# Performance work log

Hardware: AMD Instinct MI355X
Metric: run time of the kernel (lower is better)

## Reference

```python
import jax, jax.numpy as jnp
import numpy as np

LEAK = 0.9
BASE_THRESH = 1.0

@jax.custom_vjp
def spike_fn(x):
    return (x >= 0).astype(x.dtype)

def _spike_fwd(x):
    return (x >= 0).astype(x.dtype), x

def _spike_bwd(x, g):
    return (g / (1.0 + 10.0 * jnp.abs(x)) ** 2,)

spike_fn.defvjp(_spike_fwd, _spike_bwd)


def setup_inputs() -> dict:
    key = jax.random.key(0)
    k1, k2, k3, k4, k5 = jax.random.split(key, 5)
    B, T, C, NC, TDA = 256, 4096, 64, 4, 50
    kin_spikes_seq = jax.random.uniform(k1, (B, T, C), dtype=jnp.float32)
    tda_features = jax.random.normal(k2, (B, TDA), dtype=jnp.float32)
    W_spatial = jax.random.normal(k3, (NC, C), dtype=jnp.float32) * 0.125
    lateral = jnp.eye(NC, dtype=jnp.float32) * 1.1 - 0.1  # 1.0 diag, -0.1 off-diag
    W_tda = jax.random.normal(k4, (NC, TDA), dtype=jnp.float32) * 0.14
    b_tda = jnp.zeros((NC,), dtype=jnp.float32)
    return {
        "kin_spikes_seq": kin_spikes_seq,
        "tda_features": tda_features,
        "W_spatial": W_spatial,
        "lateral": lateral,
        "W_tda": W_tda,
        "b_tda": b_tda,
    }


def reference(kin_spikes_seq, tda_features, W_spatial, lateral, W_tda, b_tda):
    B, T, C = kin_spikes_seq.shape
    NC = W_spatial.shape[0]
    # dynamic threshold: base + 0.3*sigmoid(Linear(tda))  -> [B, NC]
    tda_mod = jax.nn.sigmoid(tda_features @ W_tda.T + b_tda) * 0.3
    dynamic_thresh = BASE_THRESH + tda_mod
    # project all time steps at once: (x @ W_spatial.T) @ lateral  -> [B, T, NC]
    proj = jnp.einsum("btc,nc->btn", kin_spikes_seq, W_spatial) @ lateral
    proj_t = jnp.transpose(proj, (1, 0, 2))  # [T, B, NC]

    def step(mem, cur_input):
        mem = LEAK * mem + cur_input
        spikes = spike_fn(mem - dynamic_thresh)
        mem = mem * (1.0 - spikes)
        return mem, spikes

    mem0 = jnp.zeros((B, NC), dtype=kin_spikes_seq.dtype)
    _, spikes_t = jax.lax.scan(step, mem0, proj_t)  # [T, B, NC]
    return jnp.transpose(spikes_t, (1, 0, 2))  # [B, T, NC]
```

## Files before the change

kernel.cpp:

```cpp
#include <hip/hip_runtime.h>
#include <math.h>

namespace {
constexpr int T    = 4096;
constexpr int C    = 64;
constexpr int NCH  = 4;
constexpr int TDAF = 50;
constexpr double LEAK = 0.9;
constexpr int CHUNK = 256;
constexpr int WARM  = 384;
}

__global__ __launch_bounds__(256, 2)
void lif_proj3(const float* __restrict__ x,
               const float* __restrict__ Wsp,
               const float* __restrict__ lat,
               double* __restrict__ proj,
               int B)
{
  const int tid = threadIdx.x;
  const int nb  = B >> 2;
  const int b0  = (blockIdx.x % nb) << 2;
  const int t00 = (blockIdx.x / nb) << 6;
  const int stride = B * NCH;

  const int c8 = tid & 7;
  const int rr = tid >> 3;
  const int bl = rr & 3;
  const int tl = rr >> 2;

  double wA[4][4], wB[4][4];
  #pragma unroll
  for (int j = 0; j < 4; ++j) {
    const int cA = c8 * 4 + j, cB = 32 + c8 * 4 + j;
    #pragma unroll
    for (int n = 0; n < 4; ++n) {
      double sA = 0.0, sB = 0.0;
      #pragma unroll
      for (int m = 0; m < 4; ++m) {
        sA += (double)Wsp[m * C + cA] * (double)lat[m * NCH + n];
        sB += (double)Wsp[m * C + cB] * (double)lat[m * NCH + n];
      }
      wA[j][n] = sA;
      wB[j][n] = sB;
    }
  }

  const float4* gx = reinterpret_cast<const float4*>(x);
  const size_t rowbase = (size_t)(b0 + bl) * T;

  float4 va0, vb0, va1, vb1;

#define LD(IT, VA, VB)                                              \
  {                                                                 \
    const size_t r16 = (rowbase + (size_t)(t00 + (IT) * 8 + tl)) * 16; \
    VA = gx[r16 + c8];                                              \
    VB = gx[r16 + 8 + c8];                                          \
  }

#define CS(IT, VA, VB)                                              \
  {                                                                 \
    double p0 = 0.0, p1 = 0.0, p2 = 0.0, p3 = 0.0;                  \
    p0 = fma((double)VA.x, wA[0][0], p0);                           \
    p1 = fma((double)VA.x, wA[0][1], p1);                           \
    p2 = fma((double)VA.x, wA[0][2], p2);                           \
    p3 = fma((double)VA.x, wA[0][3], p3);                           \
    p0 = fma((double)VA.y, wA[1][0], p0);                           \
    p1 = fma((double)VA.y, wA[1][1], p1);                           \
    p2 = fma((double)VA.y, wA[1][2], p2);                           \
    p3 = fma((double)VA.y, wA[1][3], p3);                           \
    p0 = fma((double)VA.z, wA[2][0], p0);                           \
    p1 = fma((double)VA.z, wA[2][1], p1);                           \
    p2 = fma((double)VA.z, wA[2][2], p2);                           \
    p3 = fma((double)VA.z, wA[2][3], p3);                           \
    p0 = fma((double)VA.w, wA[3][0], p0);                           \
    p1 = fma((double)VA.w, wA[3][1], p1);                           \
    p2 = fma((double)VA.w, wA[3][2], p2);                           \
    p3 = fma((double)VA.w, wA[3][3], p3);                           \
    p0 = fma((double)VB.x, wB[0][0], p0);                           \
    p1 = fma((double)VB.x, wB[0][1], p1);                           \
    p2 = fma((double)VB.x, wB[0][2], p2);                           \
    p3 = fma((double)VB.x, wB[0][3], p3);                           \
    p0 = fma((double)VB.y, wB[1][0], p0);                           \
    p1 = fma((double)VB.y, wB[1][1], p1);                           \
    p2 = fma((double)VB.y, wB[1][2], p2);                           \
    p3 = fma((double)VB.y, wB[1][3], p3);                           \
    p0 = fma((double)VB.z, wB[2][0], p0);                           \
    p1 = fma((double)VB.z, wB[2][1], p1);                           \
    p2 = fma((double)VB.z, wB[2][2], p2);                           \
    p3 = fma((double)VB.z, wB[2][3], p3);                           \
    p0 = fma((double)VB.w, wB[3][0], p0);                           \
    p1 = fma((double)VB.w, wB[3][1], p1);                           \
    p2 = fma((double)VB.w, wB[3][2], p2);                           \
    p3 = fma((double)VB.w, wB[3][3], p3);                           \
    p0 += __shfl_xor(p0, 1, 64); p1 += __shfl_xor(p1, 1, 64);       \
    p2 += __shfl_xor(p2, 1, 64); p3 += __shfl_xor(p3, 1, 64);       \
    p0 += __shfl_xor(p0, 2, 64); p1 += __shfl_xor(p1, 2, 64);       \
    p2 += __shfl_xor(p2, 2, 64); p3 += __shfl_xor(p3, 2, 64);       \
    p0 += __shfl_xor(p0, 4, 64); p1 += __shfl_xor(p1, 4, 64);       \
    p2 += __shfl_xor(p2, 4, 64); p3 += __shfl_xor(p3, 4, 64);       \
    if (c8 < 4) {                                                   \
      const double v = (c8 == 0) ? p0 : (c8 == 1) ? p1              \
                     : (c8 == 2) ? p2 : p3;                         \
      proj[(size_t)(t00 + (IT) * 8 + tl) * stride +                 \
           (b0 + bl) * 4 + c8] = v;                                 \
    }                                                               \
  }

  LD(0, va0, vb0)
  LD(1, va1, vb1)
  CS(0, va0, vb0)
  LD(2, va0, vb0)
  CS(1, va1, vb1)
  LD(3, va1, vb1)
  CS(2, va0, vb0)
  LD(4, va0, vb0)
  CS(3, va1, vb1)
  LD(5, va1, vb1)
  CS(4, va0, vb0)
  LD(6, va0, vb0)
  CS(5, va1, vb1)
  LD(7, va1, vb1)
  CS(6, va0, vb0)
  CS(7, va1, vb1)

#undef LD
#undef CS
}

__global__ __launch_bounds__(64, 1)
void lif_scan_chunk(const double* __restrict__ proj,
                    const float* __restrict__ tda,
                    const float* __restrict__ Wtda,
                    const float* __restrict__ btda,
                    unsigned long long* __restrict__ masks,
                    int B)
{
  const int lane = threadIdx.x;
  const int nw   = (B * NCH) >> 6;
  const int wv   = blockIdx.x % nw;
  const int ck   = blockIdx.x / nw;
  const int g    = wv * 64 + lane;
  const int b    = g >> 2, n = g & 3;
  const int stride = B * NCH;
  const int t1 = ck * CHUNK;
  const int s0 = (t1 >= WARM) ? (t1 - WARM) : 0;
  const int t2 = t1 + CHUNK;

  double z = (double)btda[n];
  #pragma unroll
  for (int j = 0; j < TDAF; ++j)
    z += (double)tda[b * TDAF + j] * (double)Wtda[n * TDAF + j];
  const double th = 1.0 + 0.3 / (1.0 + exp(-z));

  double pb[8][8];
  #pragma unroll
  for (int j2 = 0; j2 < 8; ++j2)
    #pragma unroll
    for (int e = 0; e < 8; ++e)
      pb[j2][e] = proj[(size_t)(s0 + j2 * 8 + e) * stride + g];

  double pre = 0.0;
  bool sflag = true;

  for (int t0 = s0; t0 < t2; t0 += 64) {
    unsigned lo = 0u, hi = 0u;
    #pragma unroll
    for (int j2 = 0; j2 < 8; ++j2) {
      #pragma unroll
      for (int e = 0; e < 8; ++e) {
        const int k = j2 * 8 + e;
        const double p  = pb[j2][e];
        const double ac = fma(LEAK, pre, p);
        pre   = sflag ? p : ac;
        sflag = (pre >= th);
        if (k < 32) lo |= ((unsigned)sflag) << k;
        else        hi |= ((unsigned)sflag) << (k - 32);
      }
      int tt = t0 + 64 + j2 * 8;
      tt = (tt < T) ? tt : (T - 64);
      #pragma unroll
      for (int e = 0; e < 8; ++e)
        pb[j2][e] = proj[(size_t)(tt + e) * stride + g];
    }
    if (t0 >= t1)
      masks[(size_t)g * (T / 64) + (t0 >> 6)] =
          ((unsigned long long)hi << 32) | lo;
  }
}

__global__ __launch_bounds__(256)
void lif_expand(const unsigned long long* __restrict__ masks,
                float* __restrict__ out)
{
  const int tid = threadIdx.x;
  const int b   = blockIdx.x >> 2;
  const int t0  = ((blockIdx.x & 3) << 10) + tid * 4;
  const int w   = t0 >> 6;

  unsigned long long m[4];
  #pragma unroll
  for (int n = 0; n < NCH; ++n)
    m[n] = masks[(size_t)(b * 4 + n) * (T / 64) + w];

  float4* o = reinterpret_cast<float4*>(out + ((size_t)b * T + t0) * NCH);
  #pragma unroll
  for (int j = 0; j < 4; ++j) {
    const int sh = (t0 + j) & 63;
    float4 v;
    v.x = ((m[0] >> sh) & 1ull) ? 1.0f : 0.0f;
    v.y = ((m[1] >> sh) & 1ull) ? 1.0f : 0.0f;
    v.z = ((m[2] >> sh) & 1ull) ? 1.0f : 0.0f;
    v.w = ((m[3] >> sh) & 1ull) ? 1.0f : 0.0f;
    o[j] = v;
  }
}

__global__ __launch_bounds__(128, 2)
void lif_proj(const float* __restrict__ x, const float* __restrict__ Wsp,
              const float* __restrict__ lat, double* __restrict__ proj, int B)
{
  __shared__ float  xl[32 * 76];
  __shared__ double wl[NCH * C];
  __shared__ double pl[8 * 17];

  const int tid = threadIdx.x;
  const int nb  = B >> 2;
  const int bq  = blockIdx.x % nb;
  const int tq  = blockIdx.x / nb;
  const int b0  = bq << 2;
  const int t00 = tq << 6;
  const int stride = B * NCH;

  #pragma unroll
  for (int k = 0; k < 2; ++k) {
    const int idx = tid + 128 * k;
    const int c = idx >> 2, n = idx & 3;
    double s = 0.0;
    #pragma unroll
    for (int m = 0; m < NCH; ++m)
      s += (double)Wsp[m * C + c] * (double)lat[m * NCH + n];
    wl[n * C + c] = s;
  }
  __syncthreads();

  const int n  = tid & 3;
  const int rr = tid >> 2;
  const int bb = rr >> 3, ii = rr & 7;

  double w[C];
  #pragma unroll
  for (int j = 0; j < C; ++j) w[j] = wl[n * C + j];

  const float4* gx = reinterpret_cast<const float4*>(x);

  for (int ch = 0; ch < 8; ++ch) {
    const int t0 = t00 + (ch << 3);
    __syncthreads();
    #pragma unroll
    for (int k = 0; k < 4; ++k) {
      const int f   = tid + 128 * k;
      const int row = f >> 4, c4 = f & 15;
      const int wb  = row >> 3, wi = row & 7;
      *reinterpret_cast<float4*>(&xl[row * 76 + c4 * 4]) =
          gx[((size_t)(b0 + wb) * T + (t0 + wi)) * 16 + c4];
    }
    __syncthreads();
    const float* rowp = &xl[rr * 76];
    double a0 = 0.0, a1 = 0.0;
    #pragma unroll
    for (int q = 0; q < 16; ++q) {
      const float4 v = *reinterpret_cast<const float4*>(&rowp[4 * q]);
      a0 = fma((double)v.x, w[4 * q + 0], a0);
      a1 = fma((double)v.y, w[4 * q + 1], a1);
      a0 = fma((double)v.z, w[4 * q + 2], a0);
      a1 = fma((double)v.w, w[4 * q + 3], a1);
    }
    pl[ii * 17 + bb * 4 + n] = a0 + a1;
    __syncthreads();
    {
      const int i = tid >> 4, c = tid & 15;
      proj[(size_t)(t0 + i) * stride + b0 * 4 + c] = pl[i * 17 + c];
    }
  }
}

__global__ __launch_bounds__(64)
void lif_scan_lds(const double* __restrict__ proj,
                  const float* __restrict__ tda,
                  const float* __restrict__ Wtda,
                  const float* __restrict__ btda,
                  float* __restrict__ out, int B)
{
  __shared__ float slds[64 * 65];
  const int lane = threadIdx.x;
  const int g = blockIdx.x * 64 + lane;
  const int b = g >> 2, n = g & 3;
  const int b0 = (blockIdx.x * 64) >> 2;
  const int stride = B * NCH;
  double z = (double)btda[n];
  #pragma unroll
  for (int j = 0; j < TDAF; ++j)
    z += (double)tda[b * TDAF + j] * (double)Wtda[n * TDAF + j];
  const double th = 1.0 + 0.3 / (1.0 + exp(-z));
  double pb[8][8];
  #pragma unroll
  for (int j2 = 0; j2 < 8; ++j2)
    #pragma unroll
    for (int e = 0; e < 8; ++e)
      pb[j2][e] = proj[(size_t)(j2 * 8 + e) * stride + g];
  double pre = 0.0;
  bool sflag = true;
  for (int t0 = 0; t0 < T; t0 += 64) {
    #pragma unroll
    for (int j2 = 0; j2 < 8; ++j2) {
      #pragma unroll
      for (int e = 0; e < 8; ++e) {
        const double p  = pb[j2][e];
        const double ac = fma(LEAK, pre, p);
        pre   = sflag ? p : ac;
        sflag = (pre >= th);
        slds[(j2 * 8 + e) * 65 + lane] = sflag ? 1.0f : 0.0f;
      }
      int tt = t0 + 64 + j2 * 8;
      tt = (tt < T) ? tt : (T - 64);
      #pragma unroll
      for (int e = 0; e < 8; ++e)
        pb[j2][e] = proj[(size_t)(tt + e) * stride + g];
    }
    __syncthreads();
    #pragma unroll
    for (int bb = 0; bb < 16; ++bb) {
      #pragma unroll
      for (int h = 0; h < 4; ++h) {
        const int flat = lane + 64 * h;
        const int i = flat >> 2, nn = flat & 3;
        out[((size_t)(b0 + bb) * T + (t0 + i)) * NCH + nn] =
            slds[i * 65 + bb * 4 + nn];
      }
    }
    __syncthreads();
  }
}

namespace fb {
constexpr int TT = 128, NT = T / TT, XPAD = 76, THREADS = 512;
}
__global__ __launch_bounds__(fb::THREADS, 2)
void lif_fused(const float* __restrict__ x, const float* __restrict__ tda,
               const float* __restrict__ Wsp, const float* __restrict__ lat,
               const float* __restrict__ Wtda, const float* __restrict__ btda,
               float* __restrict__ out)
{
  using namespace fb;
  __shared__ float  xl[2][TT * XPAD];
  __shared__ double wl[NCH * C];
  __shared__ double projl[TT * NCH];
  __shared__ float  spikel[TT * NCH];
  __shared__ double thl[NCH];
  const int b = blockIdx.x, tid = threadIdx.x;
  const int n = tid & 3, tl = tid >> 2;
  if (tid < NCH) {
    double z = (double)btda[tid];
    for (int j = 0; j < TDAF; ++j)
      z += (double)tda[b * TDAF + j] * (double)Wtda[tid * TDAF + j];
    thl[tid] = 1.0 + 0.3 / (1.0 + exp(-z));
  }
  if (tid < NCH * C) {
    const int c = tid >> 2, nn = tid & 3;
    double s = 0.0;
    for (int m = 0; m < NCH; ++m)
      s += (double)Wsp[m * C + c] * (double)lat[m * NCH + nn];
    wl[nn * C + c] = s;
  }
  __syncthreads();
  double w[C];
  #pragma unroll
  for (int j = 0; j < C; ++j) w[j] = wl[n * C + j];
  const double th = thl[n];
  const float4* gx = reinterpret_cast<const float4*>(x) + (size_t)b * (T * C / 4);
  float4 ra[4], rb[4];
  #pragma unroll
  for (int r = 0; r < 4; ++r) ra[r] = gx[tid + THREADS * r];
  double pre = 0.0;
  bool sflag = true;
  auto stage = [&](int buf, const float4* rr) {
    #pragma unroll
    for (int r = 0; r < 4; ++r) {
      const int f = tid + THREADS * r;
      const int t = f >> 4, c4 = (f & 15) << 2;
      *reinterpret_cast<float4*>(&xl[buf][t * XPAD + c4]) = rr[r];
    }
  };
  auto prefetch = [&](int k, float4* rr) {
    const float4* src = gx + (size_t)k * (TT * C / 4);
    #pragma unroll
    for (int r = 0; r < 4; ++r) rr[r] = src[tid + THREADS * r];
  };
  auto tilework = [&](int buf, int k) {
    __syncthreads();
    const float* row = &xl[buf][tl * XPAD];
    double a0 = 0.0, a1 = 0.0;
    #pragma unroll
    for (int q = 0; q < 16; ++q) {
      const float4 v = *reinterpret_cast<const float4*>(&row[4 * q]);
      a0 = fma((double)v.x, w[4 * q + 0], a0);
      a1 = fma((double)v.y, w[4 * q + 1], a1);
      a0 = fma((double)v.z, w[4 * q + 2], a0);
      a1 = fma((double)v.w, w[4 * q + 3], a1);
    }
    projl[tid] = a0 + a1;
    __syncthreads();
    if (tid < NCH) {
      #pragma unroll 4
      for (int t = 0; t < TT; ++t) {
        const double p  = projl[t * NCH + tid];
        const double ac = fma(LEAK, pre, p);
        pre   = sflag ? p : ac;
        sflag = (pre >= th);
        spikel[t * NCH + tid] = sflag ? 1.0f : 0.0f;
      }
    }
    __syncthreads();
    out[((size_t)b * T + (size_t)k * TT) * NCH + tid] = spikel[tid];
  };
  for (int k = 0; k < NT; k += 2) {
    stage(0, ra);
    if (k + 1 < NT) prefetch(k + 1, rb);
    tilework(0, k);
    stage(1, rb);
    if (k + 2 < NT) prefetch(k + 2, ra);
    tilework(1, k + 1);
  }
}

extern "C" void kernel_launch(void* const* d_in, const int* in_sizes, int n_in,
                              void* d_out, int out_size, void* d_ws, size_t ws_size,
                              hipStream_t stream) {
  const float* x    = (const float*)d_in[0];
  const float* tda  = (const float*)d_in[1];
  const float* Wsp  = (const float*)d_in[2];
  const float* lat  = (const float*)d_in[3];
  const float* Wtda = (const float*)d_in[4];
  const float* btda = (const float*)d_in[5];
  float* out = (float*)d_out;
  const int B = in_sizes[0] / (T * C);

  const size_t need_proj = (size_t)T * (size_t)B * NCH * sizeof(double);
  const size_t need_mask = (size_t)B * NCH * (T / 64) * sizeof(unsigned long long);

  if (ws_size >= need_proj + need_mask && (B % 4) == 0 && (B * NCH) % 64 == 0) {
    double* proj = (double*)d_ws;
    unsigned long long* masks =
        (unsigned long long*)((char*)d_ws + need_proj);
    lif_proj3<<<(B / 4) * (T / 64), 256, 0, stream>>>(x, Wsp, lat, proj, B);
    const int grid2 = (T / CHUNK) * ((B * NCH) / 64);
    lif_scan_chunk<<<grid2, 64, 0, stream>>>(proj, tda, Wtda, btda, masks, B);
    lif_expand<<<B * 4, 256, 0, stream>>>(masks, out);
  } else if (ws_size >= need_proj && (B % 4) == 0) {
    double* proj = (double*)d_ws;
    lif_proj<<<(B / 4) * (T / 64), 128, 0, stream>>>(x, Wsp, lat, proj, B);
    lif_scan_lds<<<(B * NCH) / 64, 64, 0, stream>>>(proj, tda, Wtda, btda,
                                                    out, B);
  } else {
    lif_fused<<<B, fb::THREADS, 0, stream>>>(x, tda, Wsp, lat, Wtda, btda, out);
  }
}
```

Before: 93.17 us.

## Fuse spike-mask expansion into chunked scan kernel and halve chunk size

Drops the separate mask-expansion kernel. The scan kernel now stages each 64-step spike mask word in LDS and writes the float4 output directly for its 16 batch rows. The chunk size is halved to expose more blocks. In exchange, warm-up recomputation grows relative to useful work, since the warm-up window stays at 384 steps while chunks now cover 128, and the output stores from the scan are strided across batch rows.

Result: faster. 86.35 us (-7.3%).

```diff
diff --git a/kernel.cpp b/kernel.cpp
--- a/kernel.cpp
+++ b/kernel.cpp
@@ -7,7 +7,7 @@
 constexpr int NCH  = 4;
 constexpr int TDAF = 50;
 constexpr double LEAK = 0.9;
-constexpr int CHUNK = 256;
+constexpr int CHUNK = 128;
 constexpr int WARM  = 384;
 }
 
@@ -129,19 +129,22 @@
 }
 
 __global__ __launch_bounds__(64, 1)
-void lif_scan_chunk(const double* __restrict__ proj,
+void lif_scan_fused(const double* __restrict__ proj,
                     const float* __restrict__ tda,
                     const float* __restrict__ Wtda,
                     const float* __restrict__ btda,
-                    unsigned long long* __restrict__ masks,
+                    float* __restrict__ out,
                     int B)
 {
+  __shared__ unsigned long long mlds[64];
+
   const int lane = threadIdx.x;
   const int nw   = (B * NCH) >> 6;
   const int wv   = blockIdx.x % nw;
   const int ck   = blockIdx.x / nw;
   const int g    = wv * 64 + lane;
   const int b    = g >> 2, n = g & 3;
+  const int b0s  = wv * 16;
   const int stride = B * NCH;
   const int t1 = ck * CHUNK;
   const int s0 = (t1 >= WARM) ? (t1 - WARM) : 0;
@@ -183,36 +186,26 @@
       for (int e = 0; e < 8; ++e)
         pb[j2][e] = proj[(size_t)(tt + e) * stride + g];
     }
-    if (t0 >= t1)
-      masks[(size_t)g * (T / 64) + (t0 >> 6)] =
-          ((unsigned long long)hi << 32) | lo;
-  }
-}
-
-__global__ __launch_bounds__(256)
-void lif_expand(const unsigned long long* __restrict__ masks,
-                float* __restrict__ out)
-{
-  const int tid = threadIdx.x;
-  const int b   = blockIdx.x >> 2;
-  const int t0  = ((blockIdx.x & 3) << 10) + tid * 4;
-  const int w   = t0 >> 6;
-
-  unsigned long long m[4];
-  #pragma unroll
-  for (int n = 0; n < NCH; ++n)
-    m[n] = masks[(size_t)(b * 4 + n) * (T / 64) + w];
-
-  float4* o = reinterpret_cast<float4*>(out + ((size_t)b * T + t0) * NCH);
-  #pragma unroll
-  for (int j = 0; j < 4; ++j) {
-    const int sh = (t0 + j) & 63;
-    float4 v;
-    v.x = ((m[0] >> sh) & 1ull) ? 1.0f : 0.0f;
-    v.y = ((m[1] >> sh) & 1ull) ? 1.0f : 0.0f;
-    v.z = ((m[2] >> sh) & 1ull) ? 1.0f : 0.0f;
-    v.w = ((m[3] >> sh) & 1ull) ? 1.0f : 0.0f;
-    o[j] = v;
+    if (t0 >= t1) {
+      __syncthreads();
+      mlds[lane] = ((unsigned long long)hi << 32) | lo;
+      __syncthreads();
+      #pragma unroll
+      for (int bb = 0; bb < 16; ++bb) {
+        const unsigned long long m0 = mlds[bb * 4 + 0];
+        const unsigned long long m1 = mlds[bb * 4 + 1];
+        const unsigned long long m2 = mlds[bb * 4 + 2];
+        const unsigned long long m3 = mlds[bb * 4 + 3];
+        float4 v;
+        v.x = ((m0 >> lane) & 1ull) ? 1.0f : 0.0f;
+        v.y = ((m1 >> lane) & 1ull) ? 1.0f : 0.0f;
+        v.z = ((m2 >> lane) & 1ull) ? 1.0f : 0.0f;
+        v.w = ((m3 >> lane) & 1ull) ? 1.0f : 0.0f;
+        float4* o = reinterpret_cast<float4*>(
+            out + ((size_t)(b0s + bb) * T + t0 + lane) * NCH);
+        *o = v;
+      }
+    }
   }
 }
 
@@ -447,16 +440,12 @@
   const int B = in_sizes[0] / (T * C);
 
   const size_t need_proj = (size_t)T * (size_t)B * NCH * sizeof(double);
-  const size_t need_mask = (size_t)B * NCH * (T / 64) * sizeof(unsigned long long);
-
-  if (ws_size >= need_proj + need_mask && (B % 4) == 0 && (B * NCH) % 64 == 0) {
+
+  if (ws_size >= need_proj && (B % 4) == 0 && (B * NCH) % 64 == 0) {
     double* proj = (double*)d_ws;
-    unsigned long long* masks =
-        (unsigned long long*)((char*)d_ws + need_proj);
     lif_proj3<<<(B / 4) * (T / 64), 256, 0, stream>>>(x, Wsp, lat, proj, B);
     const int grid2 = (T / CHUNK) * ((B * NCH) / 64);
-    lif_scan_chunk<<<grid2, 64, 0, stream>>>(proj, tda, Wtda, btda, masks, B);
-    lif_expand<<<B * 4, 256, 0, stream>>>(masks, out);
+    lif_scan_fused<<<grid2, 64, 0, stream>>>(proj, tda, Wtda, btda, out, B);
   } else if (ws_size >= need_proj && (B % 4) == 0) {
     double* proj = (double*)d_ws;
     lif_proj<<<(B / 4) * (T / 64), 128, 0, stream>>>(x, Wsp, lat, proj, B);
```
